# Kernel optimization log

Measured on AMD Instinct MI355X. Metric: run time of the kernel, lower is better.

Reference implementation:

```python
import jax, jax.numpy as jnp
import numpy as np

B, S, E, D = 4, 2048, 1024, 512


def setup_inputs() -> dict:
    key = jax.random.key(0)
    ks = jax.random.split(key, 7)
    s_in = 1.0 / np.sqrt(E)
    return {
        "x": jax.random.normal(ks[0], (B, S, E), dtype=jnp.float32),
        "wq": jax.random.uniform(ks[1], (E, D), jnp.float32, -s_in, s_in),
        "bq": jax.random.uniform(ks[2], (D,), jnp.float32, -s_in, s_in),
        "wk": jax.random.uniform(ks[3], (E, D), jnp.float32, -s_in, s_in),
        "bk": jax.random.uniform(ks[4], (D,), jnp.float32, -s_in, s_in),
        "wv": jax.random.uniform(ks[5], (E, D), jnp.float32, -s_in, s_in),
        "bv": jax.random.uniform(ks[6], (D,), jnp.float32, -s_in, s_in),
    }


def reference(x, wq, bq, wk, bk, wv, bv):
    # QKV projections: [B,S,E] @ [E,D] -> [B,S,D]
    q = jnp.einsum('bse,ed->bsd', x, wq) + bq
    k = jnp.einsum('bse,ed->bsd', x, wk) + bk
    v = jnp.einsum('bse,ed->bsd', x, wv) + bv
    # scores [B,S,S]
    scores = jnp.einsum('bqd,bkd->bqk', q, k)
    # causal mask applied before scaling (as in original; -inf unaffected by scale)
    causal = jnp.tril(jnp.ones((S, S), dtype=bool))
    scores = jnp.where(causal[None], scores, -jnp.inf)
    scores = scores / jnp.sqrt(jnp.float32(D))
    attn = jax.nn.softmax(scores, axis=-1)
    return jnp.einsum('bqk,bkd->bqd', attn, v)
```

## Files before the change

### kernel.cpp

```cpp
#include <hip/hip_runtime.h>
#include <math.h>


typedef __attribute__((ext_vector_type(4))) float f32x4;
typedef __attribute__((ext_vector_type(16))) float f32x16;
typedef __attribute__((ext_vector_type(8))) short bf16x8;
typedef __attribute__((ext_vector_type(8))) unsigned short u16x8;

#define B_ 4
#define S_ 2048
#define E_ 1024
#define D_ 512

__device__ __forceinline__ unsigned short f2bf(float f) {
  unsigned u = __float_as_uint(f);
  u += 0x7fffu + ((u >> 16) & 1u);
  return (unsigned short)(u >> 16);
}

__device__ __forceinline__ float bf2f(unsigned short h) {
  return __uint_as_float(((unsigned)h) << 16);
}

template<int N> __device__ __forceinline__ void wait_vm() {
  if constexpr (N == 0)      asm volatile("s_waitcnt vmcnt(0)" ::: "memory");
  else if constexpr (N == 3) asm volatile("s_waitcnt vmcnt(3)" ::: "memory");
  else if constexpr (N == 4) asm volatile("s_waitcnt vmcnt(4)" ::: "memory");
  else if constexpr (N == 5) asm volatile("s_waitcnt vmcnt(5)" ::: "memory");
  else static_assert(N != N, "unsupported vmcnt");
}


template<int ROWS, int NTHR>
__device__ __forceinline__ void stage_tile32(const unsigned short* __restrict__ g, long ld,
                                             long rowBase, int kBase,
                                             unsigned short* lds, int tid) {
  constexpr int CALLS = (ROWS * 64) / (NTHR * 16);
  #pragma unroll
  for (int i = 0; i < CALLS; ++i) {
    int idx = i * NTHR + tid;
    int row = idx >> 2, cc = idx & 3;
    int src_g = cc ^ ((row >> 1) & 3);
    __builtin_amdgcn_global_load_lds(
      (const __attribute__((address_space(1))) void*)(g + (rowBase + row) * ld + kBase + src_g * 8),
      (__attribute__((address_space(3))) void*)(lds + idx * 8),
      16, 0, 0);
  }
}

template<int MT, int NTT>
__device__ __forceinline__ void compute_tile32(const unsigned short* As, const unsigned short* Bs,
                                               int a_row0, int b_row0, int lane,
                                               f32x16 (&acc)[MT][NTT]) {
  int lr = lane & 31, lhalf = lane >> 5;
  int p = (lr >> 1) & 3;
  #pragma unroll
  for (int ki = 0; ki < 2; ++ki) {
    int slot = ((ki * 2 + lhalf) ^ p) * 8;
    bf16x8 af[MT], bf[NTT];
    #pragma unroll
    for (int mt = 0; mt < MT; ++mt)
      af[mt] = *(const bf16x8*)(As + (a_row0 + mt * 32 + lr) * 32 + slot);
    #pragma unroll
    for (int nt = 0; nt < NTT; ++nt)
      bf[nt] = *(const bf16x8*)(Bs + (b_row0 + nt * 32 + lr) * 32 + slot);
    #pragma unroll
    for (int mt = 0; mt < MT; ++mt)
      #pragma unroll
      for (int nt = 0; nt < NTT; ++nt)
        acc[mt][nt] = __builtin_amdgcn_mfma_f32_32x32x16_bf16(af[mt], bf[nt], acc[mt][nt], 0, 0, 0);
  }
}

template<int AROWS, int BROWS, int NTHR, int MT, int NTT>
__device__ __forceinline__ void mainloop32(
    const unsigned short* __restrict__ A, long lda, long rowA,
    const unsigned short* __restrict__ Bt, long ldb, long rowB,
    int nsteps, unsigned short* AsBuf, unsigned short* BsBuf,
    int tid, int lane, int a_row0, int b_row0, f32x16 (&acc)[MT][NTT]) {
  constexpr int ASZ = AROWS * 32, BSZ = BROWS * 32;
  constexpr int LPS = (AROWS * 64) / (NTHR * 16) + (BROWS * 64) / (NTHR * 16);
  unsigned short *a0 = AsBuf, *a1 = AsBuf + ASZ, *a2 = AsBuf + 2 * ASZ;
  unsigned short *b0 = BsBuf, *b1 = BsBuf + BSZ, *b2 = BsBuf + 2 * BSZ;
  stage_tile32<AROWS, NTHR>(A, lda, rowA, 0, a0, tid);
  stage_tile32<BROWS, NTHR>(Bt, ldb, rowB, 0, b0, tid);
  if (nsteps > 1) {
    stage_tile32<AROWS, NTHR>(A, lda, rowA, 32, a1, tid);
    stage_tile32<BROWS, NTHR>(Bt, ldb, rowB, 32, b1, tid);
  }
  for (int t = 0; t < nsteps; ++t) {
    if (t < nsteps - 1) wait_vm<LPS>(); else wait_vm<0>();
    __builtin_amdgcn_s_barrier();
    __builtin_amdgcn_sched_barrier(0);
    compute_tile32<MT, NTT>(a0, b0, a_row0, b_row0, lane, acc);
    if (t + 2 < nsteps) {
      stage_tile32<AROWS, NTHR>(A, lda, rowA, (t + 2) * 32, a2, tid);
      stage_tile32<BROWS, NTHR>(Bt, ldb, rowB, (t + 2) * 32, b2, tid);
    }
    unsigned short* ta = a0; a0 = a1; a1 = a2; a2 = ta;
    unsigned short* tb = b0; b0 = b1; b1 = b2; b2 = tb;
  }
}

__device__ __forceinline__ void compute_pv(const unsigned short* As, const unsigned short* Bs,
                                           int b_row0, int lane,
                                           f32x16 (&acc)[2], float& rs) {
  int lr = lane & 31, lhalf = lane >> 5;
  int p = (lr >> 1) & 3;
  #pragma unroll
  for (int ki = 0; ki < 2; ++ki) {
    int slot = ((ki * 2 + lhalf) ^ p) * 8;
    bf16x8 af = *(const bf16x8*)(As + lr * 32 + slot);
    bf16x8 bf0 = *(const bf16x8*)(Bs + (b_row0 + lr) * 32 + slot);
    bf16x8 bf1 = *(const bf16x8*)(Bs + (b_row0 + 32 + lr) * 32 + slot);
    #pragma unroll
    for (int j = 0; j < 8; ++j) rs += bf2f((unsigned short)af[j]);
    acc[0] = __builtin_amdgcn_mfma_f32_32x32x16_bf16(af, bf0, acc[0], 0, 0, 0);
    acc[1] = __builtin_amdgcn_mfma_f32_32x32x16_bf16(af, bf1, acc[1], 0, 0, 0);
  }
}

__device__ __forceinline__ void pv_mainloop(
    const unsigned short* __restrict__ A, long rowA,
    const unsigned short* __restrict__ Bt, long rowB,
    int nsteps, unsigned short* AsBuf, unsigned short* BsBuf,
    int tid, int lane, int b_row0, f32x16 (&acc)[2], float& rs) {
  constexpr int ASZ = 32 * 32, BSZ = 128 * 32;
  unsigned short *a0 = AsBuf, *a1 = AsBuf + ASZ, *a2 = AsBuf + 2 * ASZ;
  unsigned short *b0 = BsBuf, *b1 = BsBuf + BSZ, *b2 = BsBuf + 2 * BSZ;
  stage_tile32<32, 128>(A, S_, rowA, 0, a0, tid);
  stage_tile32<128, 128>(Bt, S_, rowB, 0, b0, tid);
  if (nsteps > 1) {
    stage_tile32<32, 128>(A, S_, rowA, 32, a1, tid);
    stage_tile32<128, 128>(Bt, S_, rowB, 32, b1, tid);
  }
  for (int t = 0; t < nsteps; ++t) {
    if (t < nsteps - 1) wait_vm<5>(); else wait_vm<0>();
    __builtin_amdgcn_s_barrier();
    __builtin_amdgcn_sched_barrier(0);
    compute_pv(a0, b0, b_row0, lane, acc, rs);
    if (t + 2 < nsteps) {
      stage_tile32<32, 128>(A, S_, rowA, (t + 2) * 32, a2, tid);
      stage_tile32<128, 128>(Bt, S_, rowB, (t + 2) * 32, b2, tid);
    }
    unsigned short* ta = a0; a0 = a1; a1 = a2; a2 = ta;
    unsigned short* tb = b0; b0 = b1; b1 = b2; b2 = tb;
  }
}


__global__ __launch_bounds__(256) void convert_f32_bf16(const float* __restrict__ src,
                                                        unsigned short* __restrict__ dst) {
  long i = (long)blockIdx.x * 256 + threadIdx.x;
  f32x4 a = ((const f32x4*)src)[2 * i];
  f32x4 b = ((const f32x4*)src)[2 * i + 1];
  u16x8 o;
  #pragma unroll
  for (int j = 0; j < 4; ++j) { o[j] = f2bf(a[j]); o[4 + j] = f2bf(b[j]); }
  ((u16x8*)dst)[i] = o;
}

__global__ __launch_bounds__(256) void build_wT(const float* __restrict__ wq,
                                                const float* __restrict__ wk,
                                                const float* __restrict__ wv,
                                                unsigned short* __restrict__ wbT) {
  int o = blockIdx.x * 256 + threadIdx.x;
  int n = o >> 10, k = o & 1023;
  const float* w = (n < 512) ? wq : ((n < 1024) ? wk : wv);
  int d = n & 511;
  wbT[o] = f2bf(w[(long)k * 512 + d]);
}

__global__ __launch_bounds__(256, 3) void qkv_gemm(
    const unsigned short* __restrict__ xb, const unsigned short* __restrict__ wbT,
    const float* __restrict__ bq, const float* __restrict__ bk, const float* __restrict__ bv,
    unsigned short* __restrict__ qb, unsigned short* __restrict__ kb,
    unsigned short* __restrict__ vb) {
  __shared__ unsigned short As[3][128 * 32], Bs[3][128 * 32];
  int tid = threadIdx.x, wave = tid >> 6, lane = tid & 63;
  int wm = wave >> 1, wn = wave & 1;
  int wg = blockIdx.x;
  int swz = (wg & 7) * 96 + (wg >> 3);
  int nb = swz % 12, mb = swz / 12;
  long rowA = (long)mb * 128, rowB = (long)nb * 128;
  f32x16 acc[2][2] = {};
  mainloop32<128, 128, 256, 2, 2>(xb, E_, rowA, wbT, E_, rowB, E_ / 32,
                                  &As[0][0], &Bs[0][0], tid, lane, wm * 64, wn * 64, acc);
  int lc = lane & 31, lhi = (lane >> 5) * 4;
  #pragma unroll
  for (int nt = 0; nt < 2; ++nt) {
    int n = (int)rowB + wn * 64 + nt * 32 + lc;
    int d = n & 511;
    float bias; unsigned short* dst;
    if (n < 512)       { bias = bq[d]; dst = qb; }
    else if (n < 1024) { bias = bk[d]; dst = kb; }
    else               { bias = bv[d]; dst = vb; }
    #pragma unroll
    for (int mt = 0; mt < 2; ++mt) {
      long mbase = rowA + wm * 64 + mt * 32 + lhi;
      #pragma unroll
      for (int r = 0; r < 16; ++r) {
        long m = mbase + (r & 3) + 8 * (r >> 2);
        dst[m * D_ + d] = f2bf(acc[mt][nt][r] + bias);
      }
    }
  }
}

__global__ __launch_bounds__(256) void transpose_v(const unsigned short* __restrict__ vb,
                                                   unsigned short* __restrict__ vtb) {
  int dblk = blockIdx.x;
  int sblk = blockIdx.y;
  int b = blockIdx.z;
  __shared__ unsigned short ls[64][72];
  int tid = threadIdx.x;
  int r = tid >> 3, c8 = (tid & 7) * 8;
  long d0 = (long)dblk * 64, s0 = (long)sblk * 64;
  #pragma unroll
  for (int p = 0; p < 2; ++p) {
    u16x8 v = *(const u16x8*)(vb + ((long)b * S_ + s0 + r + p * 32) * D_ + d0 + c8);
    *(u16x8*)&ls[r + p * 32][c8] = v;
  }
  __syncthreads();
  #pragma unroll
  for (int p = 0; p < 2; ++p) {
    int d = r + p * 32;
    u16x8 o;
    #pragma unroll
    for (int j = 0; j < 8; ++j) o[j] = ls[c8 + j][d];
    *(u16x8*)(vtb + ((long)b * D_ + d0 + d) * S_ + s0 + c8) = o;
  }
}

__global__ __launch_bounds__(256, 4) void scores_gemm(
    const unsigned short* __restrict__ qb, const unsigned short* __restrict__ kb,
    unsigned short* __restrict__ sc) {
  int jb = blockIdx.x, im = 31 - blockIdx.y, b = blockIdx.z;
  if (2 * jb > im) return;
  __shared__ unsigned short As[3][64 * 32], Bs[3][128 * 32];
  int tid = threadIdx.x, wave = tid >> 6, lane = tid & 63;
  int wm = wave >> 1, wn = wave & 1;
  const unsigned short* A  = qb + (long)b * S_ * D_;
  const unsigned short* Bt = kb + (long)b * S_ * D_;
  long rowA = (long)im * 64, rowB = (long)jb * 128;
  f32x16 acc[1][2] = {};
  mainloop32<64, 128, 256, 1, 2>(A, D_, rowA, Bt, D_, rowB, D_ / 32,
                                 &As[0][0], &Bs[0][0], tid, lane, wm * 32, wn * 64, acc);
  unsigned short* po = sc + (long)b * S_ * S_;
  const float cexp = 1.4426950408889634f / 22.627416997969522f;
  int lc = lane & 31, lhi = (lane >> 5) * 4;
  long mbase = rowA + wm * 32 + lhi;
  #pragma unroll
  for (int r = 0; r < 16; ++r) {
    long m = mbase + (r & 3) + 8 * (r >> 2);
    #pragma unroll
    for (int nt = 0; nt < 2; ++nt) {
      long n = rowB + wn * 64 + nt * 32 + lc;
      float p = (n <= m) ? exp2f(acc[0][nt][r] * cexp) : 0.f;
      po[m * S_ + n] = f2bf(p);
    }
  }
}

__global__ __launch_bounds__(128) void pv_gemm(
    const unsigned short* __restrict__ sc, const unsigned short* __restrict__ vtb,
    float* __restrict__ out) {
  int bn = blockIdx.x, pr = blockIdx.y, b = blockIdx.z;
  __shared__ unsigned short As[3][32 * 32], Bs[3][128 * 32];
  int tid = threadIdx.x, wave = tid >> 6, lane = tid & 63;
  const unsigned short* A  = sc  + (long)b * S_ * S_;
  const unsigned short* Bt = vtb + (long)b * D_ * S_;
  float* oo = out + (long)b * S_ * D_;
  long rowB = (long)bn * 128;
  int lc = lane & 31, lhi = (lane >> 5) * 4;
  #pragma unroll
  for (int half = 0; half < 2; ++half) {
    int bm = half ? (63 - pr) : pr;
    long rowA = (long)bm * 32;
    int nsteps = bm + 1;
    f32x16 acc[2] = {};
    float rs = 0.f;
    pv_mainloop(A, rowA, Bt, rowB, nsteps,
                &As[0][0], &Bs[0][0], tid, lane, wave * 64, acc, rs);
    float rtot = rs + __shfl_xor(rs, 32);
    #pragma unroll
    for (int r = 0; r < 16; ++r) {
      int mloc = (r & 3) + 8 * (r >> 2) + lhi;
      float inv = 1.f / __shfl(rtot, mloc);
      long m = rowA + mloc;
      #pragma unroll
      for (int nt = 0; nt < 2; ++nt) {
        long n = rowB + wave * 64 + nt * 32 + lc;
        oo[m * D_ + n] = acc[nt][r] * inv;
      }
    }
    if (half == 0) __syncthreads();
  }
}

extern "C" void kernel_launch(void* const* d_in, const int* in_sizes, int n_in,
                              void* d_out, int out_size, void* d_ws, size_t ws_size,
                              hipStream_t stream) {
  const float* x   = (const float*)d_in[0];
  const float* wq  = (const float*)d_in[1];
  const float* bq  = (const float*)d_in[2];
  const float* wk  = (const float*)d_in[3];
  const float* bk  = (const float*)d_in[4];
  const float* wv  = (const float*)d_in[5];
  const float* bv  = (const float*)d_in[6];
  float* out = (float*)d_out;

  char* ws = (char*)d_ws;
  unsigned short* xb  = (unsigned short*)(ws);
  unsigned short* wbT = (unsigned short*)(ws + 16777216);
  unsigned short* qb  = (unsigned short*)(ws + 19922944);
  unsigned short* kb  = (unsigned short*)(ws + 28311552);
  unsigned short* vb  = (unsigned short*)(ws + 36700160);
  unsigned short* vtb = (unsigned short*)(ws + 45088768);
  unsigned short* sc  = (unsigned short*)(ws + 53477376);

  convert_f32_bf16<<<dim3(4096), dim3(256), 0, stream>>>(x, xb);
  build_wT<<<dim3(6144), dim3(256), 0, stream>>>(wq, wk, wv, wbT);
  qkv_gemm<<<dim3(768), dim3(256), 0, stream>>>(xb, wbT, bq, bk, bv, qb, kb, vb);
  transpose_v<<<dim3(8, 32, 4), dim3(256), 0, stream>>>(vb, vtb);
  scores_gemm<<<dim3(16, 32, 4), dim3(256), 0, stream>>>(qb, kb, sc);
  pv_gemm<<<dim3(4, 32, 4), dim3(128), 0, stream>>>(sc, vtb, out);
}
```

Before: 124.5 us.

## Restructure PV GEMM into 64-row tiles with 4-stage pipeline and MFMA row sums

The PV kernel now uses 256-thread blocks that each handle a 64x128 output tile (2x2 waves) instead of two 32-row halves, with heaviest rows scheduled first. The mainloop moves from three to four LDS buffers, prefetching three stages ahead. The softmax row-sum is computed with an extra MFMA against a vector of ones rather than scalar bf16 adds and shuffles. This aims to raise B-tile reuse and memory latency hiding, at the cost of more LDS per block, one extra MFMA per k-step, and losing the paired-half load balancing.

```diff
diff --git a/kernel.cpp b/kernel.cpp
--- a/kernel.cpp
+++ b/kernel.cpp
@@ -27,6 +27,7 @@
   else if constexpr (N == 3) asm volatile("s_waitcnt vmcnt(3)" ::: "memory");
   else if constexpr (N == 4) asm volatile("s_waitcnt vmcnt(4)" ::: "memory");
   else if constexpr (N == 5) asm volatile("s_waitcnt vmcnt(5)" ::: "memory");
+  else if constexpr (N == 6) asm volatile("s_waitcnt vmcnt(6)" ::: "memory");
   else static_assert(N != N, "unsupported vmcnt");
 }
 
@@ -102,49 +103,54 @@
   }
 }
 
-__device__ __forceinline__ void compute_pv(const unsigned short* As, const unsigned short* Bs,
-                                           int b_row0, int lane,
-                                           f32x16 (&acc)[2], float& rs) {
+__device__ __forceinline__ void compute_pv64(const unsigned short* As, const unsigned short* Bs,
+                                             int a_row0, int b_row0, int lane, bf16x8 ones,
+                                             f32x16 (&acc)[2], f32x16& accl) {
   int lr = lane & 31, lhalf = lane >> 5;
   int p = (lr >> 1) & 3;
   #pragma unroll
   for (int ki = 0; ki < 2; ++ki) {
     int slot = ((ki * 2 + lhalf) ^ p) * 8;
-    bf16x8 af = *(const bf16x8*)(As + lr * 32 + slot);
+    bf16x8 af  = *(const bf16x8*)(As + (a_row0 + lr) * 32 + slot);
     bf16x8 bf0 = *(const bf16x8*)(Bs + (b_row0 + lr) * 32 + slot);
     bf16x8 bf1 = *(const bf16x8*)(Bs + (b_row0 + 32 + lr) * 32 + slot);
-    #pragma unroll
-    for (int j = 0; j < 8; ++j) rs += bf2f((unsigned short)af[j]);
+    accl   = __builtin_amdgcn_mfma_f32_32x32x16_bf16(af, ones, accl, 0, 0, 0);
     acc[0] = __builtin_amdgcn_mfma_f32_32x32x16_bf16(af, bf0, acc[0], 0, 0, 0);
     acc[1] = __builtin_amdgcn_mfma_f32_32x32x16_bf16(af, bf1, acc[1], 0, 0, 0);
   }
 }
 
-__device__ __forceinline__ void pv_mainloop(
+__device__ __forceinline__ void pv_mainloop64(
     const unsigned short* __restrict__ A, long rowA,
     const unsigned short* __restrict__ Bt, long rowB,
-    int nsteps, unsigned short* AsBuf, unsigned short* BsBuf,
-    int tid, int lane, int b_row0, f32x16 (&acc)[2], float& rs) {
-  constexpr int ASZ = 32 * 32, BSZ = 128 * 32;
-  unsigned short *a0 = AsBuf, *a1 = AsBuf + ASZ, *a2 = AsBuf + 2 * ASZ;
-  unsigned short *b0 = BsBuf, *b1 = BsBuf + BSZ, *b2 = BsBuf + 2 * BSZ;
-  stage_tile32<32, 128>(A, S_, rowA, 0, a0, tid);
-  stage_tile32<128, 128>(Bt, S_, rowB, 0, b0, tid);
+    int nsteps, unsigned short (*As)[64 * 32], unsigned short (*Bs)[128 * 32],
+    int tid, int lane, int a_row0, int b_row0,
+    f32x16 (&acc)[2], f32x16& accl) {
+  bf16x8 ones;
+  #pragma unroll
+  for (int j = 0; j < 8; ++j) ones[j] = (short)0x3F80;
+  stage_tile32<64, 256>(A, S_, rowA, 0, As[0], tid);
+  stage_tile32<128, 256>(Bt, S_, rowB, 0, Bs[0], tid);
   if (nsteps > 1) {
-    stage_tile32<32, 128>(A, S_, rowA, 32, a1, tid);
-    stage_tile32<128, 128>(Bt, S_, rowB, 32, b1, tid);
+    stage_tile32<64, 256>(A, S_, rowA, 32, As[1], tid);
+    stage_tile32<128, 256>(Bt, S_, rowB, 32, Bs[1], tid);
+  }
+  if (nsteps > 2) {
+    stage_tile32<64, 256>(A, S_, rowA, 64, As[2], tid);
+    stage_tile32<128, 256>(Bt, S_, rowB, 64, Bs[2], tid);
   }
   for (int t = 0; t < nsteps; ++t) {
-    if (t < nsteps - 1) wait_vm<5>(); else wait_vm<0>();
+    int rem = nsteps - t;
+    if (rem > 2)      wait_vm<6>();
+    else if (rem == 2) wait_vm<3>();
+    else               wait_vm<0>();
     __builtin_amdgcn_s_barrier();
     __builtin_amdgcn_sched_barrier(0);
-    compute_pv(a0, b0, b_row0, lane, acc, rs);
-    if (t + 2 < nsteps) {
-      stage_tile32<32, 128>(A, S_, rowA, (t + 2) * 32, a2, tid);
-      stage_tile32<128, 128>(Bt, S_, rowB, (t + 2) * 32, b2, tid);
-    }
-    unsigned short* ta = a0; a0 = a1; a1 = a2; a2 = ta;
-    unsigned short* tb = b0; b0 = b1; b1 = b2; b2 = tb;
+    compute_pv64(As[t & 3], Bs[t & 3], a_row0, b_row0, lane, ones, acc, accl);
+    if (t + 3 < nsteps) {
+      stage_tile32<64, 256>(A, S_, rowA, (t + 3) * 32, As[(t + 3) & 3], tid);
+      stage_tile32<128, 256>(Bt, S_, rowB, (t + 3) * 32, Bs[(t + 3) & 3], tid);
+    }
   }
 }
 
@@ -262,39 +268,33 @@
   }
 }
 
-__global__ __launch_bounds__(128) void pv_gemm(
+__global__ __launch_bounds__(256, 3) void pv_gemm(
     const unsigned short* __restrict__ sc, const unsigned short* __restrict__ vtb,
     float* __restrict__ out) {
-  int bn = blockIdx.x, pr = blockIdx.y, b = blockIdx.z;
-  __shared__ unsigned short As[3][32 * 32], Bs[3][128 * 32];
+  int bn = blockIdx.x, bm = 31 - blockIdx.y, b = blockIdx.z;
+  __shared__ unsigned short As[4][64 * 32], Bs[4][128 * 32];
   int tid = threadIdx.x, wave = tid >> 6, lane = tid & 63;
+  int wm = wave >> 1, wn = wave & 1;
   const unsigned short* A  = sc  + (long)b * S_ * S_;
   const unsigned short* Bt = vtb + (long)b * D_ * S_;
+  long rowA = (long)bm * 64, rowB = (long)bn * 128;
+  int nsteps = 2 * (bm + 1);
+  f32x16 acc[2] = {};
+  f32x16 accl = {};
+  pv_mainloop64(A, rowA, Bt, rowB, nsteps, As, Bs, tid, lane,
+                wm * 32, wn * 64, acc, accl);
   float* oo = out + (long)b * S_ * D_;
-  long rowB = (long)bn * 128;
   int lc = lane & 31, lhi = (lane >> 5) * 4;
-  #pragma unroll
-  for (int half = 0; half < 2; ++half) {
-    int bm = half ? (63 - pr) : pr;
-    long rowA = (long)bm * 32;
-    int nsteps = bm + 1;
-    f32x16 acc[2] = {};
-    float rs = 0.f;
-    pv_mainloop(A, rowA, Bt, rowB, nsteps,
-                &As[0][0], &Bs[0][0], tid, lane, wave * 64, acc, rs);
-    float rtot = rs + __shfl_xor(rs, 32);
-    #pragma unroll
-    for (int r = 0; r < 16; ++r) {
-      int mloc = (r & 3) + 8 * (r >> 2) + lhi;
-      float inv = 1.f / __shfl(rtot, mloc);
-      long m = rowA + mloc;
-      #pragma unroll
-      for (int nt = 0; nt < 2; ++nt) {
-        long n = rowB + wave * 64 + nt * 32 + lc;
-        oo[m * D_ + n] = acc[nt][r] * inv;
-      }
-    }
-    if (half == 0) __syncthreads();
+  long mbase = rowA + wm * 32 + lhi;
+  #pragma unroll
+  for (int r = 0; r < 16; ++r) {
+    long m = mbase + (r & 3) + 8 * (r >> 2);
+    float inv = 1.f / accl[r];
+    #pragma unroll
+    for (int nt = 0; nt < 2; ++nt) {
+      long n = rowB + wn * 64 + nt * 32 + lc;
+      oo[m * D_ + n] = acc[nt][r] * inv;
+    }
   }
 }
 
@@ -324,5 +324,5 @@
   qkv_gemm<<<dim3(768), dim3(256), 0, stream>>>(xb, wbT, bq, bk, bv, qb, kb, vb);
   transpose_v<<<dim3(8, 32, 4), dim3(256), 0, stream>>>(vb, vtb);
   scores_gemm<<<dim3(16, 32, 4), dim3(256), 0, stream>>>(qb, kb, sc);
-  pv_gemm<<<dim3(4, 32, 4), dim3(128), 0, stream>>>(sc, vtb, out);
-}
+  pv_gemm<<<dim3(4, 32, 4), dim3(256), 0, stream>>>(sc, vtb, out);
+}
```

After: 122.3 us. About the same (-1.8%).
